# Kernel optimization log

Measured on AMD Instinct MI355X. Metric: run time of the kernel, lower is better.

Reference implementation:

```python
import jax, jax.numpy as jnp
import numpy as np

B, L, E, H = 64, 512, 128, 256


def setup_inputs() -> dict:
    key = jax.random.key(0)
    ks = jax.random.split(key, 16)
    s = 0.05
    return {
        "embedded_inputs": jax.random.normal(ks[0], (B, L, E), jnp.float32),
        "decoder_input": jax.random.normal(ks[1], (B, E), jnp.float32),
        "h0": jax.random.normal(ks[2], (B, H), jnp.float32),
        "c0": jax.random.normal(ks[3], (B, H), jnp.float32),
        "context": jax.random.normal(ks[4], (B, L, H), jnp.float32),
        # LSTM cell params
        "Wi": jax.random.normal(ks[5], (4 * H, E), jnp.float32) * s,
        "bi": jnp.zeros((4 * H,), jnp.float32),
        "Wh": jax.random.normal(ks[6], (4 * H, H), jnp.float32) * s,
        "bh": jnp.zeros((4 * H,), jnp.float32),
        # hidden_out: Linear(2H -> H)
        "Wo": jax.random.normal(ks[7], (H, 2 * H), jnp.float32) * s,
        "bo": jnp.zeros((H,), jnp.float32),
        # attention params: input_linear(H->H), context conv1d(H->H,k=1), V [H]
        "Wa_in": jax.random.normal(ks[8], (H, H), jnp.float32) * s,
        "ba_in": jnp.zeros((H,), jnp.float32),
        "Wa_ctx": jax.random.normal(ks[9], (H, H), jnp.float32) * s,
        "ba_ctx": jnp.zeros((H,), jnp.float32),
        "V": jax.random.normal(ks[10], (H,), jnp.float32) * s,
    }


def reference(embedded_inputs, decoder_input, h0, c0, context,
              Wi, bi, Wh, bh, Wo, bo, Wa_in, ba_in, Wa_ctx, ba_ctx, V):
    # Precompute projected context once (Conv1d with kernel 1 == per-position linear): [B,L,H]
    ctx_proj = jnp.einsum('blh,gh->blg', context, Wa_ctx) + ba_ctx

    def step(carry, _):
        dec_in, h, c, mask = carry
        gates = dec_in @ Wi.T + bi + h @ Wh.T + bh              # [B,4H]
        i_g, f_g, g_g, o_g = jnp.split(gates, 4, axis=1)
        i_g = jax.nn.sigmoid(i_g)
        f_g = jax.nn.sigmoid(f_g)
        g_g = jnp.tanh(g_g)
        o_g = jax.nn.sigmoid(o_g)
        c_t = f_g * c + i_g * g_g
        h_t = o_g * jnp.tanh(c_t)
        # attention
        inp = h_t @ Wa_in.T + ba_in                              # [B,H]
        scores = jnp.einsum('h,blh->bl', V, jnp.tanh(inp[:, None, :] + ctx_proj))
        scores = jnp.where(mask == 0, -jnp.inf, scores)
        alpha = jax.nn.softmax(scores, axis=1)                   # [B,L]
        att_hidden = jnp.einsum('bl,blh->bh', alpha, ctx_proj)
        hidden_t = jnp.tanh(jnp.concatenate([att_hidden, h_t], axis=1) @ Wo.T + bo)
        # pointer: argmax over still-available positions
        masked_outs = alpha * mask
        idx = jnp.argmax(masked_outs, axis=1)                    # [B]
        one_hot = jax.nn.one_hot(idx, L, dtype=mask.dtype)
        mask_next = mask * (1.0 - one_hot)
        dec_next = jnp.take_along_axis(embedded_inputs, idx[:, None, None], axis=1)[:, 0]
        return (dec_next, hidden_t, c_t, mask_next), (alpha, idx)

    mask0 = jnp.ones((B, L), jnp.float32)
    carry0 = (decoder_input, h0, c0, mask0)
    (dec_f, h_f, c_f, _), (alphas, ptrs) = jax.lax.scan(step, carry0, None, length=L)
    outputs = jnp.transpose(alphas, (1, 0, 2))                   # [B,L,L]
    pointers = jnp.transpose(ptrs, (1, 0))                       # [B,L]
    return outputs, pointers, h_f, c_f
```

## Files before the change

### kernel.cpp

```cpp
#include <hip/hip_runtime.h>
#include <math.h>

#define SCOPE __HIP_MEMORY_SCOPE_AGENT

constexpr int Bn = 64, Ln = 512, En = 128, Hn = 256, Tn = 512;
constexpr int NBLK = 512, NTHR = 256;
constexpr int CTX_LD = 256, XPAD = 384, UPAD = 520;

constexpr int OFF_CTX = 0;
constexpr int OFF_SCR = 64 * CTX_LD;
constexpr int OFF_INP = OFF_SCR + 2048;
constexpr int OFF_SS  = OFF_INP + 256;
constexpr int OFF_ES  = OFF_SS + 64;
constexpr int OFF_MK  = OFF_ES + 64;
constexpr int OFF_VS  = OFF_MK + 64;
constexpr int OFF_GS  = OFF_VS + 256;
constexpr int OFF_ST  = OFF_GS + 128;
constexpr int OFF_BA  = OFF_ST + 64;
constexpr int OFF_HTL = OFF_BA + 256;
constexpr int SMEM_FL = OFF_HTL + 32;

constexpr size_t PTR_OFF = (size_t)Bn * Ln * Ln;
constexpr size_t HF_OFF  = PTR_OFF + (size_t)Bn * Ln;
constexpr size_t CF_OFF  = HF_OFF + (size_t)Bn * Hn;

constexpr int GQ_HT    = 0;
constexpr int GQ_HID   = 512;
constexpr int GQ_ATT   = 1024;
constexpr int GQ_STATS = 5120;
constexpr int GQ_INPP  = 5184;
constexpr int GQ_STRIDE = 5184 + 8192;

__device__ __forceinline__ float fast_tanh(float x) {
  const float e = __expf(2.0f * x);
  return 1.0f - __fdividef(2.0f, 1.0f + e);
}
__device__ __forceinline__ float sigmoidf_(float x) {
  return 1.0f / (1.0f + expf(-x));
}
__device__ __forceinline__ void llc_storef(float* p, float v) {
  __hip_atomic_store(p, v, __ATOMIC_RELAXED, SCOPE);
}
__device__ __forceinline__ float4 llc_ld4(const float* p) {
  float4 r;
  asm volatile("global_load_dwordx4 %0, %1, off sc0 sc1\n\ts_waitcnt vmcnt(0)"
               : "=&v"(r) : "v"(p) : "memory");
  return r;
}
__device__ __forceinline__ void llc_ld4x4(const float* p0, const float* p1,
                                          const float* p2, const float* p3,
                                          float4& a, float4& b, float4& c, float4& d) {
  asm volatile(
      "global_load_dwordx4 %0, %4, off sc0 sc1\n\t"
      "global_load_dwordx4 %1, %5, off sc0 sc1\n\t"
      "global_load_dwordx4 %2, %6, off sc0 sc1\n\t"
      "global_load_dwordx4 %3, %7, off sc0 sc1\n\t"
      "s_waitcnt vmcnt(0)"
      : "=&v"(a), "=&v"(b), "=&v"(c), "=&v"(d)
      : "v"(p0), "v"(p1), "v"(p2), "v"(p3) : "memory");
}
__device__ __forceinline__ void llc_ld5(const float* p0, const float* p1,
                                        const float* p2, const float* p3,
                                        const float* p4,
                                        float4& a, float4& b, float4& c,
                                        float4& d, float4& e) {
  asm volatile(
      "global_load_dwordx4 %0, %5, off sc0 sc1\n\t"
      "global_load_dwordx4 %1, %6, off sc0 sc1\n\t"
      "global_load_dwordx4 %2, %7, off sc0 sc1\n\t"
      "global_load_dwordx4 %3, %8, off sc0 sc1\n\t"
      "global_load_dwordx4 %4, %9, off sc0 sc1\n\t"
      "s_waitcnt vmcnt(0)"
      : "=&v"(a), "=&v"(b), "=&v"(c), "=&v"(d), "=&v"(e)
      : "v"(p0), "v"(p1), "v"(p2), "v"(p3), "v"(p4) : "memory");
}

__device__ __forceinline__ void group_barrier16(unsigned* flags_g, int j, unsigned tgt) {
  asm volatile("s_waitcnt vmcnt(0)" ::: "memory");
  __syncthreads();
  if (threadIdx.x == 0)
    __hip_atomic_store(&flags_g[j * 32], tgt, __ATOMIC_RELAXED, SCOPE);
  if (threadIdx.x < 16) {
    long spins = 0;
    while (__hip_atomic_load(&flags_g[threadIdx.x * 32], __ATOMIC_RELAXED, SCOPE) < tgt) {
      __builtin_amdgcn_s_sleep(1);
      if (++spins > 50000000L) __builtin_trap();
    }
  }
  __syncthreads();
  asm volatile("" ::: "memory");
}

#define DOT4(acc, w4, x4) \
  acc = fmaf((w4).x, (x4).x, fmaf((w4).y, (x4).y, fmaf((w4).z, (x4).z, fmaf((w4).w, (x4).w, (acc)))))

__global__ void __launch_bounds__(NTHR, 2)
decoder_main(const float* __restrict__ emb, const float* __restrict__ dec0,
             const float* __restrict__ h0,  const float* __restrict__ c0,
             const float* __restrict__ ctxg,const float* __restrict__ Wi,
             const float* __restrict__ bi,  const float* __restrict__ Wh,
             const float* __restrict__ bh,  const float* __restrict__ Wo,
             const float* __restrict__ bo,  const float* __restrict__ Wain,
             const float* __restrict__ bain,const float* __restrict__ Wactx,
             const float* __restrict__ bactx,const float* __restrict__ Vv,
             float* __restrict__ out, unsigned* __restrict__ flags,
             float* __restrict__ wsd)
{
  extern __shared__ float sm[];
  float* ctx    = sm + OFF_CTX;
  float* scr    = sm + OFF_SCR;
  float* x_s    = sm + OFF_SCR;
  float* inp_s  = sm + OFF_INP;
  float* s_s    = sm + OFF_SS;
  float* e_s    = sm + OFF_ES;
  float* mask_s = sm + OFF_MK;
  float* V_s    = sm + OFF_VS;
  float* gsum   = sm + OFF_GS;
  float* stats_s= sm + OFF_ST;
  float* bain_s = sm + OFF_BA;
  float* htl_s  = sm + OFF_HTL;

  const int tid = threadIdx.x, bid = blockIdx.x;
  const int gq = bid >> 4, j = bid & 15;
  const int bbj = j >> 3, ck = j & 7;
  const int b_ctx = gq * 2 + bbj;
  const int l0 = ck * 64;

  const int team = tid >> 2, seg4 = tid & 3;
  const int gteam = team >> 4, hloc = team & 15;
  const int r_abs = gteam * 256 + j * 16 + hloc;
  const int r16loc = tid >> 4, seg16 = tid & 15;
  const int r16 = j * 16 + r16loc;
  const int hq = tid & 63, lg = tid >> 6;

  unsigned* flags_g = flags + gq * (16 * 32);
  float* wsg = wsd + (size_t)gq * GQ_STRIDE;

  const float* wiRow = Wi + (size_t)r_abs * En;
  const float* whRow = Wh + (size_t)r_abs * Hn;
  const float* waRow = Wain + (size_t)tid * Hn + j * 16;
  const float* woRow = Wo + (size_t)r16 * (2 * Hn);
  const float bias_g = bi[r_abs] + bh[r_abs];
  const float bo_r = bo[r16];

  float cst = 0.0f;
  if (tid < 32) cst = c0[(size_t)(gq * 2 + (tid >> 4)) * Hn + j * 16 + (tid & 15)];

  if (tid < 64) mask_s[tid] = 1.0f;
  V_s[tid] = Vv[tid];
  bain_s[tid] = bain[tid];

  {
    const int gc = tid & 31, lgi = tid >> 5;
    float acc[8][8];
    #pragma unroll
    for (int a2 = 0; a2 < 8; ++a2)
      #pragma unroll
      for (int b2 = 0; b2 < 8; ++b2) acc[a2][b2] = 0.0f;
    float* stg_c = scr;
    float* stg_w = scr + 256;
    for (int kc = 0; kc < 64; ++kc) {
      __syncthreads();
      {
        const int k = tid >> 6, l = tid & 63;
        stg_c[k * 64 + l] = ctxg[((size_t)(b_ctx * Ln + l0 + l)) * Hn + kc * 4 + k];
      }
      #pragma unroll
      for (int it = 0; it < 4; ++it) {
        const int i = tid + it * 256;
        const int k = i >> 8, gg = i & 255;
        stg_w[k * 256 + gg] = Wactx[(size_t)gg * Hn + kc * 4 + k];
      }
      __syncthreads();
      #pragma unroll
      for (int kk = 0; kk < 4; ++kk) {
        float cl[8], wgt[8];
        #pragma unroll
        for (int jj = 0; jj < 8; ++jj) cl[jj] = stg_c[kk * 64 + lgi * 8 + jj];
        #pragma unroll
        for (int jj = 0; jj < 8; ++jj) wgt[jj] = stg_w[kk * 256 + gc * 8 + jj];
        #pragma unroll
        for (int li = 0; li < 8; ++li)
          #pragma unroll
          for (int gi = 0; gi < 8; ++gi)
            acc[li][gi] = fmaf(cl[li], wgt[gi], acc[li][gi]);
      }
    }
    __syncthreads();
    #pragma unroll
    for (int li = 0; li < 8; ++li)
      #pragma unroll
      for (int gi = 0; gi < 8; ++gi)
        ctx[(lgi * 8 + li) * CTX_LD + gc * 8 + gi] = acc[li][gi] + bactx[gc * 8 + gi];
  }
  __syncthreads();

  unsigned tgt = 1;
  int w0 = 0, w1 = 0;

  for (int t = 0; t < Tn; ++t) {
    {
      if (tid < 128) {
        const int bbx = tid >> 6, h4 = tid & 63;
        float4 v;
        if (t == 0) v = *(const float4*)&h0[(size_t)(gq * 2 + bbx) * Hn + h4 * 4];
        else        v = llc_ld4(wsg + GQ_HID + bbx * 256 + h4 * 4);
        *(float4*)&x_s[bbx * XPAD + 128 + h4 * 4] = v;
      } else if (tid < 192) {
        const int i2 = tid - 128, bbx = i2 >> 5, k4 = i2 & 31;
        const int gb = gq * 2 + bbx;
        float4 v;
        if (t == 0) v = *(const float4*)&dec0[(size_t)gb * En + k4 * 4];
        else {
          const int wsel = (bbx == 0) ? w0 : w1;
          v = *(const float4*)&emb[((size_t)gb * Ln + wsel) * En + k4 * 4];
        }
        *(float4*)&x_s[bbx * XPAD + k4 * 4] = v;
      }
      __syncthreads();
      {
        float acc0 = 0.0f, acc1 = 0.0f;
        #pragma unroll
        for (int k = 0; k < 8; ++k) {
          const float4 w4 = *(const float4*)&wiRow[k * 16 + seg4 * 4];
          const float4 xa = *(const float4*)&x_s[k * 16 + seg4 * 4];
          const float4 xb = *(const float4*)&x_s[XPAD + k * 16 + seg4 * 4];
          DOT4(acc0, w4, xa);
          DOT4(acc1, w4, xb);
        }
        #pragma unroll
        for (int k = 0; k < 16; ++k) {
          const float4 w4 = *(const float4*)&whRow[k * 16 + seg4 * 4];
          const float4 xa = *(const float4*)&x_s[128 + k * 16 + seg4 * 4];
          const float4 xb = *(const float4*)&x_s[XPAD + 128 + k * 16 + seg4 * 4];
          DOT4(acc0, w4, xa);
          DOT4(acc1, w4, xb);
        }
        acc0 += __shfl_xor(acc0, 1, 64);
        acc0 += __shfl_xor(acc0, 2, 64);
        acc1 += __shfl_xor(acc1, 1, 64);
        acc1 += __shfl_xor(acc1, 2, 64);
        if (seg4 == 0) {
          gsum[team] = acc0 + bias_g;
          gsum[64 + team] = acc1 + bias_g;
        }
      }
      __syncthreads();
      if (tid < 32) {
        const int bbx = tid >> 4, hx = tid & 15;
        const float iv = gsum[bbx * 64 + hx];
        const float fv = gsum[bbx * 64 + 16 + hx];
        const float gv = gsum[bbx * 64 + 32 + hx];
        const float ov = gsum[bbx * 64 + 48 + hx];
        const float cn = sigmoidf_(fv) * cst + sigmoidf_(iv) * tanhf(gv);
        const float htv = sigmoidf_(ov) * tanhf(cn);
        cst = cn;
        htl_s[bbx * 16 + hx] = htv;
        llc_storef(wsg + GQ_HT + bbx * 256 + j * 16 + hx, htv);
        if (t == Tn - 1) out[CF_OFF + (size_t)(gq * 2 + bbx) * Hn + j * 16 + hx] = cn;
      }
      __syncthreads();
      {
        float a0 = 0.0f, a1 = 0.0f;
        #pragma unroll
        for (int k = 0; k < 4; ++k) {
          const float4 w4 = *(const float4*)&waRow[k * 4];
          const float4 xa = *(const float4*)&htl_s[k * 4];
          const float4 xb = *(const float4*)&htl_s[16 + k * 4];
          DOT4(a0, w4, xa);
          DOT4(a1, w4, xb);
        }
        llc_storef(wsg + GQ_INPP + tid * 16 + j, a0);
        llc_storef(wsg + GQ_INPP + 4096 + tid * 16 + j, a1);
      }
    }
    group_barrier16(flags_g, j, tgt++);

    {
      {
        const float* ib = wsg + GQ_INPP + bbj * 4096 + tid * 16;
        float4 a0, a1, a2, a3;
        llc_ld4x4(ib, ib + 4, ib + 8, ib + 12, a0, a1, a2, a3);
        const float s01 = ((a0.x + a0.y) + (a0.z + a0.w)) + ((a1.x + a1.y) + (a1.z + a1.w));
        const float s23 = ((a2.x + a2.y) + (a2.z + a2.w)) + ((a3.x + a3.y) + (a3.z + a3.w));
        inp_s[tid] = s01 + s23 + bain_s[tid];
      }
      __syncthreads();
      {
        const float4 in4 = *(const float4*)&inp_s[hq * 4];
        const float4 v4  = *(const float4*)&V_s[hq * 4];
        #pragma unroll
        for (int pass = 0; pass < 2; ++pass) {
          const int lb = pass * 32 + lg * 8;
          float p0, p1, p2, p3, p4, p5, p6, p7;
          #define SCORE_P(dst, li)                                           \
            {                                                                \
              const float4 c4 = *(const float4*)&ctx[(lb + (li)) * CTX_LD + hq * 4]; \
              float p;                                                       \
              p = v4.x * fast_tanh(in4.x + c4.x);                            \
              p = fmaf(v4.y, fast_tanh(in4.y + c4.y), p);                    \
              p = fmaf(v4.z, fast_tanh(in4.z + c4.z), p);                    \
              p = fmaf(v4.w, fast_tanh(in4.w + c4.w), p);                    \
              dst = p;                                                       \
            }
          SCORE_P(p0, 0) SCORE_P(p1, 1) SCORE_P(p2, 2) SCORE_P(p3, 3)
          SCORE_P(p4, 4) SCORE_P(p5, 5) SCORE_P(p6, 6) SCORE_P(p7, 7)
          #undef SCORE_P
          const bool hi32 = (hq & 32) != 0;
          float s, q0, q1, q2, q3, r0, r1, t0;
          s = hi32 ? p0 : p4; s = __shfl_xor(s, 32, 64); q0 = (hi32 ? p4 : p0) + s;
          s = hi32 ? p1 : p5; s = __shfl_xor(s, 32, 64); q1 = (hi32 ? p5 : p1) + s;
          s = hi32 ? p2 : p6; s = __shfl_xor(s, 32, 64); q2 = (hi32 ? p6 : p2) + s;
          s = hi32 ? p3 : p7; s = __shfl_xor(s, 32, 64); q3 = (hi32 ? p7 : p3) + s;
          const bool hi16 = (hq & 16) != 0;
          s = hi16 ? q0 : q2; s = __shfl_xor(s, 16, 64); r0 = (hi16 ? q2 : q0) + s;
          s = hi16 ? q1 : q3; s = __shfl_xor(s, 16, 64); r1 = (hi16 ? q3 : q1) + s;
          const bool hi8 = (hq & 8) != 0;
          s = hi8 ? r0 : r1; s = __shfl_xor(s, 8, 64); t0 = (hi8 ? r1 : r0) + s;
          t0 += __shfl_xor(t0, 4, 64);
          t0 += __shfl_xor(t0, 2, 64);
          t0 += __shfl_xor(t0, 1, 64);
          if ((hq & 7) == 0) {
            const int l = lb + ((hq >> 3) & 7);
            s_s[l] = (mask_s[l] == 0.0f) ? -INFINITY : t0;
          }
        }
      }
      __syncthreads();
      if (tid < 64) {
        const float sv = s_s[tid];
        const float e = expf(sv);
        e_s[tid] = e;
        float ssum = e;
        #pragma unroll
        for (int m = 1; m < 64; m <<= 1) ssum += __shfl_xor(ssum, m, 64);
        float cv = sv; int ci = tid;
        #pragma unroll
        for (int m = 1; m < 64; m <<= 1) {
          const float ov = __shfl_xor(cv, m, 64);
          const int   oi = __shfl_xor(ci, m, 64);
          if (ov > cv || (ov == cv && oi < ci)) { cv = ov; ci = oi; }
        }
        if (tid == 0) {
          float* stb = wsg + GQ_STATS + (bbj * 8 + ck) * 4;
          llc_storef(stb + 0, ssum);
          llc_storef(stb + 1, cv);
          llc_storef(stb + 2, (float)(l0 + ci));
        }
      }
      __syncthreads();
      {
        float p0 = 0, p1 = 0, p2 = 0, p3 = 0;
        #pragma unroll
        for (int pass = 0; pass < 2; ++pass) {
          #pragma unroll
          for (int li = 0; li < 8; ++li) {
            const int l = pass * 32 + lg * 8 + li;
            const float ev = e_s[l];
            const float4 c4 = *(const float4*)&ctx[l * CTX_LD + hq * 4];
            p0 = fmaf(ev, c4.x, p0);
            p1 = fmaf(ev, c4.y, p1);
            p2 = fmaf(ev, c4.z, p2);
            p3 = fmaf(ev, c4.w, p3);
          }
        }
        __syncthreads();
        *(float4*)&scr[lg * 256 + hq * 4] = make_float4(p0, p1, p2, p3);
      }
      __syncthreads();
      {
        float a = 0.0f;
        #pragma unroll
        for (int r2 = 0; r2 < 4; ++r2) a += scr[r2 * 256 + tid];
        llc_storef(wsg + GQ_ATT + (bbj * 8 + ck) * 256 + tid, a);
      }
    }
    group_barrier16(flags_g, j, tgt++);

    {
      float4 sum4 = make_float4(0, 0, 0, 0), htv4 = make_float4(0, 0, 0, 0);
      if (tid >= 128 && tid < 144) {
        const float4 st = llc_ld4(wsg + GQ_STATS + (tid - 128) * 4);
        *(float4*)&stats_s[(tid - 128) * 4] = st;
      }
      if (tid < 128) {
        const int bbx = tid >> 6, h4 = tid & 63;
        const float* ab = wsg + GQ_ATT + bbx * 2048 + h4 * 4;
        float4 a0, a1, a2, a3, b0, b1, b2, b3;
        llc_ld4x4(ab, ab + 256, ab + 512, ab + 768, a0, a1, a2, a3);
        sum4.x = ((a0.x + a1.x) + (a2.x + a3.x));
        sum4.y = ((a0.y + a1.y) + (a2.y + a3.y));
        sum4.z = ((a0.z + a1.z) + (a2.z + a3.z));
        sum4.w = ((a0.w + a1.w) + (a2.w + a3.w));
        llc_ld5(ab + 1024, ab + 1280, ab + 1536, ab + 1792,
                wsg + GQ_HT + bbx * 256 + h4 * 4, b0, b1, b2, b3, htv4);
        sum4.x += ((b0.x + b1.x) + (b2.x + b3.x));
        sum4.y += ((b0.y + b1.y) + (b2.y + b3.y));
        sum4.z += ((b0.z + b1.z) + (b2.z + b3.z));
        sum4.w += ((b0.w + b1.w) + (b2.w + b3.w));
      }
      __syncthreads();
      float Sb[2]; int wq[2];
      #pragma unroll
      for (int bb = 0; bb < 2; ++bb) {
        float Ssum = 0.0f;
        #pragma unroll
        for (int c2 = 0; c2 < 8; ++c2) Ssum += stats_s[(bb * 8 + c2) * 4];
        Sb[bb] = Ssum;
        float bv = stats_s[(bb * 8 + 0) * 4 + 1];
        int bI = (int)stats_s[(bb * 8 + 0) * 4 + 2];
        #pragma unroll
        for (int c2 = 1; c2 < 8; ++c2) {
          const float v2 = stats_s[(bb * 8 + c2) * 4 + 1];
          const int i2 = (int)stats_s[(bb * 8 + c2) * 4 + 2];
          if (v2 > bv || (v2 == bv && i2 < bI)) { bv = v2; bI = i2; }
        }
        wq[bb] = bI;
      }
      const float Sown = (bbj == 0) ? Sb[0] : Sb[1];
      const int wown = (bbj == 0) ? wq[0] : wq[1];
      if (tid < 16) {
        const float4 e4 = *(const float4*)&e_s[tid * 4];
        *(float4*)&out[(size_t)b_ctx * Ln * Ln + (size_t)t * Ln + l0 + tid * 4] =
            make_float4(e4.x / Sown, e4.y / Sown, e4.z / Sown, e4.w / Sown);
      }
      if (tid == 0) {
        if (wown >= l0 && wown < l0 + 64) mask_s[wown - l0] = 0.0f;
        if (ck == 0) out[PTR_OFF + (size_t)b_ctx * Ln + t] = (float)wown;
      }
      if (tid < 128) {
        const int bbx = tid >> 6, h4 = tid & 63;
        const float Sx = (bbx == 0) ? Sb[0] : Sb[1];
        *(float4*)&scr[bbx * UPAD + h4 * 4] =
            make_float4(sum4.x / Sx, sum4.y / Sx, sum4.z / Sx, sum4.w / Sx);
        *(float4*)&scr[bbx * UPAD + 256 + h4 * 4] = htv4;
      }
      __syncthreads();
      {
        float a0 = 0.0f, a1 = 0.0f;
        #pragma unroll
        for (int k = 0; k < 8; ++k) {
          const float4 w4 = *(const float4*)&woRow[k * 64 + seg16 * 4];
          const float4 xa = *(const float4*)&scr[k * 64 + seg16 * 4];
          const float4 xb = *(const float4*)&scr[UPAD + k * 64 + seg16 * 4];
          DOT4(a0, w4, xa);
          DOT4(a1, w4, xb);
        }
        a0 += __shfl_xor(a0, 1, 64);
        a0 += __shfl_xor(a0, 2, 64);
        a0 += __shfl_xor(a0, 4, 64);
        a0 += __shfl_xor(a0, 8, 64);
        a1 += __shfl_xor(a1, 1, 64);
        a1 += __shfl_xor(a1, 2, 64);
        a1 += __shfl_xor(a1, 4, 64);
        a1 += __shfl_xor(a1, 8, 64);
        if (seg16 == 0) {
          const float hv0 = tanhf(a0 + bo_r);
          const float hv1 = tanhf(a1 + bo_r);
          llc_storef(wsg + GQ_HID + r16, hv0);
          llc_storef(wsg + GQ_HID + 256 + r16, hv1);
          if (t == Tn - 1) {
            out[HF_OFF + (size_t)(gq * 2 + 0) * Hn + r16] = hv0;
            out[HF_OFF + (size_t)(gq * 2 + 1) * Hn + r16] = hv1;
          }
        }
      }
      w0 = wq[0]; w1 = wq[1];
    }
    group_barrier16(flags_g, j, tgt++);
  }
}

extern "C" void kernel_launch(void* const* d_in, const int* in_sizes, int n_in,
                              void* d_out, int out_size, void* d_ws, size_t ws_size,
                              hipStream_t stream) {
  (void)in_sizes; (void)n_in; (void)out_size; (void)ws_size;
  (void)hipFuncSetAttribute(reinterpret_cast<const void*>(decoder_main),
                            hipFuncAttributeMaxDynamicSharedMemorySize, SMEM_FL * 4);
  (void)hipMemsetAsync(d_ws, 0, 65536, stream);

  const float* emb   = (const float*)d_in[0];
  const float* dec0  = (const float*)d_in[1];
  const float* h0    = (const float*)d_in[2];
  const float* c0    = (const float*)d_in[3];
  const float* ctxg  = (const float*)d_in[4];
  const float* Wi    = (const float*)d_in[5];
  const float* bi    = (const float*)d_in[6];
  const float* Wh    = (const float*)d_in[7];
  const float* bh    = (const float*)d_in[8];
  const float* Wo    = (const float*)d_in[9];
  const float* bo    = (const float*)d_in[10];
  const float* Wain  = (const float*)d_in[11];
  const float* bain  = (const float*)d_in[12];
  const float* Wactx = (const float*)d_in[13];
  const float* bactx = (const float*)d_in[14];
  const float* V     = (const float*)d_in[15];

  unsigned* flags = (unsigned*)d_ws;
  float* wsd = (float*)((char*)d_ws + 65536);

  decoder_main<<<NBLK, NTHR, SMEM_FL * 4, stream>>>(
      emb, dec0, h0, c0, ctxg, Wi, bi, Wh, bh, Wo, bo, Wain, bain, Wactx, bactx, V,
      (float*)d_out, flags, wsd);
}
```

Before: 11.23 ms.

## Compute hidden_out redundantly per block to drop one grid-group barrier per step

Each block now computes the full 256-row Wo projection for both batches locally, right after the attention barrier, instead of splitting rows across the 16 blocks and exchanging results through global memory. This removes the third group barrier per timestep and the global round-trip for the hidden state. The loop is restructured so step t finishes the previous step's epilogue, and the h_t buffer is double-buffered to avoid races. In exchange, each block does 16x more Wo work per step (a 512-length dot product per thread, reading Wo rows from global/cache).

```diff
diff --git a/kernel.cpp b/kernel.cpp
--- a/kernel.cpp
+++ b/kernel.cpp
@@ -18,14 +18,15 @@
 constexpr int OFF_ST  = OFF_GS + 128;
 constexpr int OFF_BA  = OFF_ST + 64;
 constexpr int OFF_HTL = OFF_BA + 256;
-constexpr int SMEM_FL = OFF_HTL + 32;
+constexpr int OFF_BO  = OFF_HTL + 32;
+constexpr int OFF_HID = OFF_BO + 256;
+constexpr int SMEM_FL = OFF_HID + 512;
 
 constexpr size_t PTR_OFF = (size_t)Bn * Ln * Ln;
 constexpr size_t HF_OFF  = PTR_OFF + (size_t)Bn * Ln;
 constexpr size_t CF_OFF  = HF_OFF + (size_t)Bn * Hn;
 
 constexpr int GQ_HT    = 0;
-constexpr int GQ_HID   = 512;
 constexpr int GQ_ATT   = 1024;
 constexpr int GQ_STATS = 5120;
 constexpr int GQ_INPP  = 5184;
@@ -58,21 +59,6 @@
       "s_waitcnt vmcnt(0)"
       : "=&v"(a), "=&v"(b), "=&v"(c), "=&v"(d)
       : "v"(p0), "v"(p1), "v"(p2), "v"(p3) : "memory");
-}
-__device__ __forceinline__ void llc_ld5(const float* p0, const float* p1,
-                                        const float* p2, const float* p3,
-                                        const float* p4,
-                                        float4& a, float4& b, float4& c,
-                                        float4& d, float4& e) {
-  asm volatile(
-      "global_load_dwordx4 %0, %5, off sc0 sc1\n\t"
-      "global_load_dwordx4 %1, %6, off sc0 sc1\n\t"
-      "global_load_dwordx4 %2, %7, off sc0 sc1\n\t"
-      "global_load_dwordx4 %3, %8, off sc0 sc1\n\t"
-      "global_load_dwordx4 %4, %9, off sc0 sc1\n\t"
-      "s_waitcnt vmcnt(0)"
-      : "=&v"(a), "=&v"(b), "=&v"(c), "=&v"(d), "=&v"(e)
-      : "v"(p0), "v"(p1), "v"(p2), "v"(p3), "v"(p4) : "memory");
 }
 
 __device__ __forceinline__ void group_barrier16(unsigned* flags_g, int j, unsigned tgt) {
@@ -119,6 +105,8 @@
   float* stats_s= sm + OFF_ST;
   float* bain_s = sm + OFF_BA;
   float* htl_s  = sm + OFF_HTL;
+  float* bo_s   = sm + OFF_BO;
+  float* hid_s  = sm + OFF_HID;
 
   const int tid = threadIdx.x, bid = blockIdx.x;
   const int gq = bid >> 4, j = bid & 15;
@@ -129,8 +117,6 @@
   const int team = tid >> 2, seg4 = tid & 3;
   const int gteam = team >> 4, hloc = team & 15;
   const int r_abs = gteam * 256 + j * 16 + hloc;
-  const int r16loc = tid >> 4, seg16 = tid & 15;
-  const int r16 = j * 16 + r16loc;
   const int hq = tid & 63, lg = tid >> 6;
 
   unsigned* flags_g = flags + gq * (16 * 32);
@@ -139,9 +125,8 @@
   const float* wiRow = Wi + (size_t)r_abs * En;
   const float* whRow = Wh + (size_t)r_abs * Hn;
   const float* waRow = Wain + (size_t)tid * Hn + j * 16;
-  const float* woRow = Wo + (size_t)r16 * (2 * Hn);
+  const float* woRow = Wo + (size_t)tid * (2 * Hn);
   const float bias_g = bi[r_abs] + bh[r_abs];
-  const float bo_r = bo[r16];
 
   float cst = 0.0f;
   if (tid < 32) cst = c0[(size_t)(gq * 2 + (tid >> 4)) * Hn + j * 16 + (tid & 15)];
@@ -149,6 +134,7 @@
   if (tid < 64) mask_s[tid] = 1.0f;
   V_s[tid] = Vv[tid];
   bain_s[tid] = bain[tid];
+  bo_s[tid] = bo[tid];
 
   {
     const int gc = tid & 31, lgi = tid >> 5;
@@ -196,26 +182,108 @@
   __syncthreads();
 
   unsigned tgt = 1;
-  int w0 = 0, w1 = 0;
-
-  for (int t = 0; t < Tn; ++t) {
-    {
+
+  for (int t = 0; t <= Tn; ++t) {
+    int wq0 = 0, wq1 = 0;
+    if (t > 0) {
+      const int php = (t & 1) ^ 1;
+      float4 asum = make_float4(0, 0, 0, 0);
       if (tid < 128) {
-        const int bbx = tid >> 6, h4 = tid & 63;
-        float4 v;
-        if (t == 0) v = *(const float4*)&h0[(size_t)(gq * 2 + bbx) * Hn + h4 * 4];
-        else        v = llc_ld4(wsg + GQ_HID + bbx * 256 + h4 * 4);
-        *(float4*)&x_s[bbx * XPAD + 128 + h4 * 4] = v;
-      } else if (tid < 192) {
-        const int i2 = tid - 128, bbx = i2 >> 5, k4 = i2 & 31;
+        const int bbx = tid >> 6, q = tid & 63;
+        const float* ab = wsg + GQ_ATT + bbx * 2048 + q * 4;
+        float4 a0, a1, a2, a3, b0, b1, b2, b3;
+        llc_ld4x4(ab, ab + 256, ab + 512, ab + 768, a0, a1, a2, a3);
+        llc_ld4x4(ab + 1024, ab + 1280, ab + 1536, ab + 1792, b0, b1, b2, b3);
+        asum.x = ((a0.x + a1.x) + (a2.x + a3.x)) + ((b0.x + b1.x) + (b2.x + b3.x));
+        asum.y = ((a0.y + a1.y) + (a2.y + a3.y)) + ((b0.y + b1.y) + (b2.y + b3.y));
+        asum.z = ((a0.z + a1.z) + (a2.z + a3.z)) + ((b0.z + b1.z) + (b2.z + b3.z));
+        asum.w = ((a0.w + a1.w) + (a2.w + a3.w)) + ((b0.w + b1.w) + (b2.w + b3.w));
+      } else {
+        const int tid2 = tid - 128;
+        const int bbx = tid2 >> 6, h4 = tid2 & 63;
+        const float4 hv = llc_ld4(wsg + GQ_HT + php * 512 + bbx * 256 + h4 * 4);
+        *(float4*)&scr[bbx * UPAD + 256 + h4 * 4] = hv;
+        if (tid2 < 16) {
+          const float4 st = llc_ld4(wsg + GQ_STATS + tid2 * 4);
+          *(float4*)&stats_s[tid2 * 4] = st;
+        }
+      }
+      __syncthreads();
+      float Sb[2]; int wq[2];
+      #pragma unroll
+      for (int bb = 0; bb < 2; ++bb) {
+        float Ssum = 0.0f;
+        #pragma unroll
+        for (int c2 = 0; c2 < 8; ++c2) Ssum += stats_s[(bb * 8 + c2) * 4];
+        Sb[bb] = Ssum;
+        float bv = stats_s[(bb * 8 + 0) * 4 + 1];
+        int bI = (int)stats_s[(bb * 8 + 0) * 4 + 2];
+        #pragma unroll
+        for (int c2 = 1; c2 < 8; ++c2) {
+          const float v2 = stats_s[(bb * 8 + c2) * 4 + 1];
+          const int i2 = (int)stats_s[(bb * 8 + c2) * 4 + 2];
+          if (v2 > bv || (v2 == bv && i2 < bI)) { bv = v2; bI = i2; }
+        }
+        wq[bb] = bI;
+      }
+      wq0 = wq[0]; wq1 = wq[1];
+      const float Sown = (bbj == 0) ? Sb[0] : Sb[1];
+      const int wown = (bbj == 0) ? wq[0] : wq[1];
+      if (tid < 16) {
+        const float4 e4 = *(const float4*)&e_s[tid * 4];
+        *(float4*)&out[(size_t)b_ctx * Ln * Ln + (size_t)(t - 1) * Ln + l0 + tid * 4] =
+            make_float4(e4.x / Sown, e4.y / Sown, e4.z / Sown, e4.w / Sown);
+      }
+      if (tid == 0) {
+        if (wown >= l0 && wown < l0 + 64) mask_s[wown - l0] = 0.0f;
+        if (ck == 0) out[PTR_OFF + (size_t)b_ctx * Ln + (t - 1)] = (float)wown;
+      }
+      if (tid < 128) {
+        const int bbx = tid >> 6, q = tid & 63;
+        const float Sx = (bbx == 0) ? Sb[0] : Sb[1];
+        *(float4*)&scr[bbx * UPAD + q * 4] =
+            make_float4(asum.x / Sx, asum.y / Sx, asum.z / Sx, asum.w / Sx);
+      }
+      __syncthreads();
+      {
+        float acc0 = 0.0f, acc1 = 0.0f;
+        #pragma unroll 8
+        for (int k = 0; k < 128; ++k) {
+          const float4 w4 = *(const float4*)&woRow[k * 4];
+          const float4 xa = *(const float4*)&scr[k * 4];
+          const float4 xb = *(const float4*)&scr[UPAD + k * 4];
+          DOT4(acc0, w4, xa);
+          DOT4(acc1, w4, xb);
+        }
+        const float h0v = tanhf(acc0 + bo_s[tid]);
+        const float h1v = tanhf(acc1 + bo_s[tid]);
+        hid_s[tid] = h0v;
+        hid_s[256 + tid] = h1v;
+        if (t == Tn) {
+          out[HF_OFF + (size_t)(gq * 2 + 0) * Hn + tid] = h0v;
+          out[HF_OFF + (size_t)(gq * 2 + 1) * Hn + tid] = h1v;
+        }
+      }
+    }
+
+    if (t < Tn) {
+      __syncthreads();
+      if (tid < 64) {
+        const int bbx = tid >> 5, k4 = tid & 31;
         const int gb = gq * 2 + bbx;
         float4 v;
         if (t == 0) v = *(const float4*)&dec0[(size_t)gb * En + k4 * 4];
         else {
-          const int wsel = (bbx == 0) ? w0 : w1;
+          const int wsel = (bbx == 0) ? wq0 : wq1;
           v = *(const float4*)&emb[((size_t)gb * Ln + wsel) * En + k4 * 4];
         }
         *(float4*)&x_s[bbx * XPAD + k4 * 4] = v;
+      } else if (tid < 192) {
+        const int tid2 = tid - 64, bbx = tid2 >> 6, h4 = tid2 & 63;
+        float4 v;
+        if (t == 0) v = *(const float4*)&h0[(size_t)(gq * 2 + bbx) * Hn + h4 * 4];
+        else        v = *(const float4*)&hid_s[bbx * 256 + h4 * 4];
+        *(float4*)&x_s[bbx * XPAD + 128 + h4 * 4] = v;
       }
       __syncthreads();
       {
@@ -256,7 +324,7 @@
         const float htv = sigmoidf_(ov) * tanhf(cn);
         cst = cn;
         htl_s[bbx * 16 + hx] = htv;
-        llc_storef(wsg + GQ_HT + bbx * 256 + j * 16 + hx, htv);
+        llc_storef(wsg + GQ_HT + (t & 1) * 512 + bbx * 256 + j * 16 + hx, htv);
         if (t == Tn - 1) out[CF_OFF + (size_t)(gq * 2 + bbx) * Hn + j * 16 + hx] = cn;
       }
       __syncthreads();
@@ -273,10 +341,8 @@
         llc_storef(wsg + GQ_INPP + tid * 16 + j, a0);
         llc_storef(wsg + GQ_INPP + 4096 + tid * 16 + j, a1);
       }
-    }
-    group_barrier16(flags_g, j, tgt++);
-
-    {
+      group_barrier16(flags_g, j, tgt++);
+
       {
         const float* ib = wsg + GQ_INPP + bbj * 4096 + tid * 16;
         float4 a0, a1, a2, a3;
@@ -374,100 +440,8 @@
         for (int r2 = 0; r2 < 4; ++r2) a += scr[r2 * 256 + tid];
         llc_storef(wsg + GQ_ATT + (bbj * 8 + ck) * 256 + tid, a);
       }
+      group_barrier16(flags_g, j, tgt++);
     }
-    group_barrier16(flags_g, j, tgt++);
-
-    {
-      float4 sum4 = make_float4(0, 0, 0, 0), htv4 = make_float4(0, 0, 0, 0);
-      if (tid >= 128 && tid < 144) {
-        const float4 st = llc_ld4(wsg + GQ_STATS + (tid - 128) * 4);
-        *(float4*)&stats_s[(tid - 128) * 4] = st;
-      }
-      if (tid < 128) {
-        const int bbx = tid >> 6, h4 = tid & 63;
-        const float* ab = wsg + GQ_ATT + bbx * 2048 + h4 * 4;
-        float4 a0, a1, a2, a3, b0, b1, b2, b3;
-        llc_ld4x4(ab, ab + 256, ab + 512, ab + 768, a0, a1, a2, a3);
-        sum4.x = ((a0.x + a1.x) + (a2.x + a3.x));
-        sum4.y = ((a0.y + a1.y) + (a2.y + a3.y));
-        sum4.z = ((a0.z + a1.z) + (a2.z + a3.z));
-        sum4.w = ((a0.w + a1.w) + (a2.w + a3.w));
-        llc_ld5(ab + 1024, ab + 1280, ab + 1536, ab + 1792,
-                wsg + GQ_HT + bbx * 256 + h4 * 4, b0, b1, b2, b3, htv4);
-        sum4.x += ((b0.x + b1.x) + (b2.x + b3.x));
-        sum4.y += ((b0.y + b1.y) + (b2.y + b3.y));
-        sum4.z += ((b0.z + b1.z) + (b2.z + b3.z));
-        sum4.w += ((b0.w + b1.w) + (b2.w + b3.w));
-      }
-      __syncthreads();
-      float Sb[2]; int wq[2];
-      #pragma unroll
-      for (int bb = 0; bb < 2; ++bb) {
-        float Ssum = 0.0f;
-        #pragma unroll
-        for (int c2 = 0; c2 < 8; ++c2) Ssum += stats_s[(bb * 8 + c2) * 4];
-        Sb[bb] = Ssum;
-        float bv = stats_s[(bb * 8 + 0) * 4 + 1];
-        int bI = (int)stats_s[(bb * 8 + 0) * 4 + 2];
-        #pragma unroll
-        for (int c2 = 1; c2 < 8; ++c2) {
-          const float v2 = stats_s[(bb * 8 + c2) * 4 + 1];
-          const int i2 = (int)stats_s[(bb * 8 + c2) * 4 + 2];
-          if (v2 > bv || (v2 == bv && i2 < bI)) { bv = v2; bI = i2; }
-        }
-        wq[bb] = bI;
-      }
-      const float Sown = (bbj == 0) ? Sb[0] : Sb[1];
-      const int wown = (bbj == 0) ? wq[0] : wq[1];
-      if (tid < 16) {
-        const float4 e4 = *(const float4*)&e_s[tid * 4];
-        *(float4*)&out[(size_t)b_ctx * Ln * Ln + (size_t)t * Ln + l0 + tid * 4] =
-            make_float4(e4.x / Sown, e4.y / Sown, e4.z / Sown, e4.w / Sown);
-      }
-      if (tid == 0) {
-        if (wown >= l0 && wown < l0 + 64) mask_s[wown - l0] = 0.0f;
-        if (ck == 0) out[PTR_OFF + (size_t)b_ctx * Ln + t] = (float)wown;
-      }
-      if (tid < 128) {
-        const int bbx = tid >> 6, h4 = tid & 63;
-        const float Sx = (bbx == 0) ? Sb[0] : Sb[1];
-        *(float4*)&scr[bbx * UPAD + h4 * 4] =
-            make_float4(sum4.x / Sx, sum4.y / Sx, sum4.z / Sx, sum4.w / Sx);
-        *(float4*)&scr[bbx * UPAD + 256 + h4 * 4] = htv4;
-      }
-      __syncthreads();
-      {
-        float a0 = 0.0f, a1 = 0.0f;
-        #pragma unroll
-        for (int k = 0; k < 8; ++k) {
-          const float4 w4 = *(const float4*)&woRow[k * 64 + seg16 * 4];
-          const float4 xa = *(const float4*)&scr[k * 64 + seg16 * 4];
-          const float4 xb = *(const float4*)&scr[UPAD + k * 64 + seg16 * 4];
-          DOT4(a0, w4, xa);
-          DOT4(a1, w4, xb);
-        }
-        a0 += __shfl_xor(a0, 1, 64);
-        a0 += __shfl_xor(a0, 2, 64);
-        a0 += __shfl_xor(a0, 4, 64);
-        a0 += __shfl_xor(a0, 8, 64);
-        a1 += __shfl_xor(a1, 1, 64);
-        a1 += __shfl_xor(a1, 2, 64);
-        a1 += __shfl_xor(a1, 4, 64);
-        a1 += __shfl_xor(a1, 8, 64);
-        if (seg16 == 0) {
-          const float hv0 = tanhf(a0 + bo_r);
-          const float hv1 = tanhf(a1 + bo_r);
-          llc_storef(wsg + GQ_HID + r16, hv0);
-          llc_storef(wsg + GQ_HID + 256 + r16, hv1);
-          if (t == Tn - 1) {
-            out[HF_OFF + (size_t)(gq * 2 + 0) * Hn + r16] = hv0;
-            out[HF_OFF + (size_t)(gq * 2 + 1) * Hn + r16] = hv1;
-          }
-        }
-      }
-      w0 = wq[0]; w1 = wq[1];
-    }
-    group_barrier16(flags_g, j, tgt++);
   }
 }
 
```

Result: slower. 22.13 ms (+97.1%).
